# Optimization experiments

Measured on AMD Instinct MI355X. Metric: run time of the kernel, lower is better.

## Reference

```python
import jax, jax.numpy as jnp
import numpy as np

H = 1024  # hidden_size


def setup_inputs() -> dict:
    key = jax.random.key(0)
    ks = jax.random.split(key, 8)
    B, S = 32, 2048
    scale_w = 1.0 / np.sqrt(H)
    scale_u = 1.0 / np.sqrt(2 * H)
    return {
        "encoder_annotations": jax.random.normal(ks[0], (B, S, 2 * H), dtype=jnp.float32),
        "decoder_prev_hidden": jax.random.normal(ks[1], (1, B, H), dtype=jnp.float32),
        "W_w": jax.random.uniform(ks[2], (H, H), jnp.float32, -scale_w, scale_w),
        "W_b": jax.random.uniform(ks[3], (H,), jnp.float32, -scale_w, scale_w),
        "U_w": jax.random.uniform(ks[4], (H, 2 * H), jnp.float32, -scale_u, scale_u),
        "U_b": jax.random.uniform(ks[5], (H,), jnp.float32, -scale_u, scale_u),
        "V_w": jax.random.uniform(ks[6], (1, H), jnp.float32, -scale_w, scale_w),
        "V_b": jax.random.uniform(ks[7], (1,), jnp.float32, -scale_w, scale_w),
    }


def reference(encoder_annotations, decoder_prev_hidden, W_w, W_b, U_w, U_b, V_w, V_b):
    # decoder_prev_hidden: [1, B, H] -> [B, 1, H]
    dh = jnp.transpose(decoder_prev_hidden, (1, 0, 2))
    # W(dh): [B, 1, H]; U(enc): [B, S, H]; broadcast add over S
    wq = jnp.einsum("boh,kh->bok", dh, W_w) + W_b
    uk = jnp.einsum("bsd,kd->bsk", encoder_annotations, U_w) + U_b
    act = jnp.tanh(wq + uk)  # [B, S, H]
    # V(act): [B, S, 1] -> scores [B, 1, S]
    scores = (jnp.einsum("bsh,oh->bso", act, V_w) + V_b).transpose(0, 2, 1)
    weights = jax.nn.softmax(scores, axis=2)  # [B, 1, S]
    context = jnp.einsum("bos,sd->bod", weights[:, 0:1].squeeze(1)[:, None, :].squeeze(1)[:, None, :], encoder_annotations) if False else jnp.matmul(weights, encoder_annotations)  # [B, 1, 2H]
    return context
```

## Files before the change

kernel.cpp:

```cpp
#include <hip/hip_runtime.h>
#include <hip/hip_bf16.h>

#define H_  1024
#define B_  32
#define S_  2048
#define K2_ 2048

typedef __attribute__((ext_vector_type(8))) short short8;
typedef __attribute__((ext_vector_type(4))) float floatx4;

__device__ __forceinline__ unsigned short f2bf(float x) {
    unsigned int u = __float_as_uint(x);
    u += 0x7fffu + ((u >> 16) & 1u);
    return (unsigned short)(u >> 16);
}

__device__ __forceinline__ float fast_tanh(float x) {
    float e = __expf(2.0f * x);
    return 1.0f - 2.0f / (e + 1.0f);
}

__global__ __launch_bounds__(256)
void wq_k(const float* __restrict__ dh, const float* __restrict__ Ww,
          const float* __restrict__ Wb, const float* __restrict__ Ub,
          float* __restrict__ wqbuf)
{
    const int b = blockIdx.x;
    const int tid = threadIdx.x;
    __shared__ float dhs[H_];
    for (int h = tid; h < H_; h += 256) dhs[h] = dh[b * H_ + h];
    __syncthreads();
    for (int n = tid; n < H_; n += 256) {
        const float4* row = (const float4*)(Ww + (size_t)n * H_);
        float acc = 0.f;
        #pragma unroll 4
        for (int h4 = 0; h4 < H_ / 4; h4++) {
            float4 wv = row[h4];
            acc += wv.x * dhs[h4 * 4 + 0] + wv.y * dhs[h4 * 4 + 1]
                 + wv.z * dhs[h4 * 4 + 2] + wv.w * dhs[h4 * 4 + 3];
        }
        wqbuf[b * H_ + n] = acc + Wb[n] + Ub[n];
    }
}

__global__ __launch_bounds__(256)
void gemm_scores(const float* __restrict__ enc, const float* __restrict__ Uw,
                 const float* __restrict__ wqbuf, const float* __restrict__ Vw,
                 float* __restrict__ partial)
{
    const int b   = blockIdx.z;
    const int mt  = blockIdx.x;
    const int nt  = blockIdx.y;
    const int tid = threadIdx.x;
    const int wave = tid >> 6;
    const int lane = tid & 63;

    __shared__ unsigned short As[128][32];
    __shared__ unsigned short Bs[128][32];
    __shared__ float sc[2][128];

    const float* Ab = enc + ((size_t)b * S_ + (size_t)mt * 128) * K2_;
    const float* Bb = Uw + (size_t)nt * 128 * K2_;

    floatx4 acc[4][4];
    #pragma unroll
    for (int i = 0; i < 4; i++)
        #pragma unroll
        for (int j = 0; j < 4; j++)
            acc[i][j] = (floatx4){0.f, 0.f, 0.f, 0.f};

    const int wm  = (wave & 1) * 64;
    const int wn  = (wave >> 1) * 64;
    const int l15 = lane & 15;
    const int kq  = (lane >> 4) * 8;

    for (int ks = 0; ks < K2_; ks += 32) {
        #pragma unroll
        for (int i = 0; i < 4; i++) {
            int lin = tid + 256 * i;
            int row = lin >> 3;
            int kk  = (lin & 7) << 2;
            float4 av = *(const float4*)(Ab + (size_t)row * K2_ + ks + kk);
            float4 bv = *(const float4*)(Bb + (size_t)row * K2_ + ks + kk);
            ushort4 a4 = { f2bf(av.x), f2bf(av.y), f2bf(av.z), f2bf(av.w) };
            ushort4 b4 = { f2bf(bv.x), f2bf(bv.y), f2bf(bv.z), f2bf(bv.w) };
            *(ushort4*)&As[row][kk] = a4;
            *(ushort4*)&Bs[row][kk] = b4;
        }
        __syncthreads();

        short8 af[4], bfr[4];
        #pragma unroll
        for (int t = 0; t < 4; t++) {
            af[t]  = *(const short8*)&As[wm + t * 16 + l15][kq];
            bfr[t] = *(const short8*)&Bs[wn + t * 16 + l15][kq];
        }
        #pragma unroll
        for (int tm = 0; tm < 4; tm++)
            #pragma unroll
            for (int tn = 0; tn < 4; tn++)
                acc[tm][tn] = __builtin_amdgcn_mfma_f32_16x16x32_bf16(
                    af[tm], bfr[tn], acc[tm][tn], 0, 0, 0);
        __syncthreads();
    }

    float rs[4][4];
    #pragma unroll
    for (int tm = 0; tm < 4; tm++)
        #pragma unroll
        for (int r = 0; r < 4; r++) rs[tm][r] = 0.f;

    #pragma unroll
    for (int tn = 0; tn < 4; tn++) {
        int ng = nt * 128 + wn + tn * 16 + l15;
        float vw = Vw[ng];
        float wv = wqbuf[b * H_ + ng];
        #pragma unroll
        for (int tm = 0; tm < 4; tm++)
            #pragma unroll
            for (int r = 0; r < 4; r++)
                rs[tm][r] += vw * fast_tanh(acc[tm][tn][r] + wv);
    }
    #pragma unroll
    for (int tm = 0; tm < 4; tm++)
        #pragma unroll
        for (int r = 0; r < 4; r++) {
            float v = rs[tm][r];
            v += __shfl_xor(v, 1, 64);
            v += __shfl_xor(v, 2, 64);
            v += __shfl_xor(v, 4, 64);
            v += __shfl_xor(v, 8, 64);
            rs[tm][r] = v;
        }
    if (l15 == 0) {
        int q = lane >> 4;
        #pragma unroll
        for (int tm = 0; tm < 4; tm++)
            #pragma unroll
            for (int r = 0; r < 4; r++)
                sc[wave >> 1][wm + tm * 16 + q * 4 + r] = rs[tm][r];
    }
    __syncthreads();
    if (tid < 128)
        partial[(size_t)(b * 8 + nt) * S_ + mt * 128 + tid] = sc[0][tid] + sc[1][tid];
}

__global__ __launch_bounds__(256)
void softmax_k(const float* __restrict__ partial, float* __restrict__ weights)
{
    const int b = blockIdx.x;
    const int tid = threadIdx.x;
    __shared__ float scores[S_];
    __shared__ float redm[4], reds[4];

    for (int s = tid; s < S_; s += 256) {
        float v = 0.f;
        #pragma unroll
        for (int nt = 0; nt < 8; nt++) v += partial[(size_t)(b * 8 + nt) * S_ + s];
        scores[s] = v;
    }
    __syncthreads();

    float m = -1e30f;
    for (int s = tid; s < S_; s += 256) m = fmaxf(m, scores[s]);
    #pragma unroll
    for (int off = 32; off > 0; off >>= 1) m = fmaxf(m, __shfl_xor(m, off, 64));
    if ((tid & 63) == 0) redm[tid >> 6] = m;
    __syncthreads();
    m = fmaxf(fmaxf(redm[0], redm[1]), fmaxf(redm[2], redm[3]));

    float sum = 0.f;
    for (int s = tid; s < S_; s += 256) {
        float e = __expf(scores[s] - m);
        scores[s] = e;
        sum += e;
    }
    #pragma unroll
    for (int off = 32; off > 0; off >>= 1) sum += __shfl_xor(sum, off, 64);
    if ((tid & 63) == 0) reds[tid >> 6] = sum;
    __syncthreads();
    sum = reds[0] + reds[1] + reds[2] + reds[3];
    float inv = 1.0f / sum;
    for (int s = tid; s < S_; s += 256) weights[b * S_ + s] = scores[s] * inv;
}

__global__ __launch_bounds__(256)
void context_k(const float* __restrict__ enc, const float* __restrict__ weights,
               float* __restrict__ out)
{
    const int b = blockIdx.y;
    const int d = blockIdx.x * 256 + threadIdx.x;
    const int tid = threadIdx.x;
    __shared__ float w[S_];
    for (int s = tid; s < S_; s += 256) w[s] = weights[b * S_ + s];
    __syncthreads();

    const float* e = enc + (size_t)b * S_ * K2_ + d;
    float a0 = 0.f, a1 = 0.f, a2 = 0.f, a3 = 0.f;
    for (int s = 0; s < S_; s += 4) {
        a0 += w[s + 0] * e[(size_t)(s + 0) * K2_];
        a1 += w[s + 1] * e[(size_t)(s + 1) * K2_];
        a2 += w[s + 2] * e[(size_t)(s + 2) * K2_];
        a3 += w[s + 3] * e[(size_t)(s + 3) * K2_];
    }
    out[b * K2_ + d] = (a0 + a1) + (a2 + a3);
}

extern "C" void kernel_launch(void* const* d_in, const int* in_sizes, int n_in,
                              void* d_out, int out_size, void* d_ws, size_t ws_size,
                              hipStream_t stream)
{
    const float* enc = (const float*)d_in[0];
    const float* dh  = (const float*)d_in[1];
    const float* Ww  = (const float*)d_in[2];
    const float* Wb  = (const float*)d_in[3];
    const float* Uw  = (const float*)d_in[4];
    const float* Ub  = (const float*)d_in[5];
    const float* Vw  = (const float*)d_in[6];
    float* out = (float*)d_out;

    float* wqbuf   = (float*)d_ws;
    float* partial = wqbuf + B_ * H_;
    float* weights = partial + B_ * 8 * S_;

    wq_k<<<dim3(B_), dim3(256), 0, stream>>>(dh, Ww, Wb, Ub, wqbuf);
    gemm_scores<<<dim3(16, 8, B_), dim3(256), 0, stream>>>(enc, Uw, wqbuf, Vw, partial);
    softmax_k<<<dim3(B_), dim3(256), 0, stream>>>(partial, weights);
    context_k<<<dim3(8, B_), dim3(256), 0, stream>>>(enc, weights, out);
}
```

Baseline: 1.436 ms.

## Pre-convert operands to bf16, load via direct global-to-LDS, split context over S

Adds a pass that converts the encoder annotations and U weights to bf16 in workspace, then runs the score GEMM on bf16 inputs, loading tiles straight into LDS with global_load_lds. This removes the per-block fp32 loads and conversions, which were repeated across the 8 N-tiles. The context kernel is split over S chunks with float4 loads and a separate reduction kernel, giving more parallelism, and wq_k gets a wider grid. The trade-off is an extra full pass over the encoder (read fp32, write bf16), larger workspace needs, and a fallback to the old fp32 path when the workspace is too small.

```diff
diff --git a/kernel.cpp b/kernel.cpp
--- a/kernel.cpp
+++ b/kernel.cpp
@@ -8,6 +8,7 @@
 
 typedef __attribute__((ext_vector_type(8))) short short8;
 typedef __attribute__((ext_vector_type(4))) float floatx4;
+typedef __attribute__((ext_vector_type(8))) unsigned short ushortx8;
 
 __device__ __forceinline__ unsigned short f2bf(float x) {
     unsigned int u = __float_as_uint(x);
@@ -20,33 +21,154 @@
     return 1.0f - 2.0f / (e + 1.0f);
 }
 
+__device__ __forceinline__ void gload_lds16(const void* g, void* l) {
+    __builtin_amdgcn_global_load_lds(
+        (const __attribute__((address_space(1))) unsigned int*)g,
+        (__attribute__((address_space(3))) unsigned int*)l, 16, 0, 0);
+}
+
+__global__ __launch_bounds__(256)
+void cvt_bf16_k(const float* __restrict__ in, unsigned short* __restrict__ out, long long n8)
+{
+    long long i = (long long)blockIdx.x * 256 + threadIdx.x;
+    long long stride = (long long)gridDim.x * 256;
+    for (; i < n8; i += stride) {
+        const float4* p = (const float4*)in + i * 2;
+        float4 a = p[0], b = p[1];
+        ushortx8 o = { f2bf(a.x), f2bf(a.y), f2bf(a.z), f2bf(a.w),
+                       f2bf(b.x), f2bf(b.y), f2bf(b.z), f2bf(b.w) };
+        *(ushortx8*)(out + i * 8) = o;
+    }
+}
+
 __global__ __launch_bounds__(256)
 void wq_k(const float* __restrict__ dh, const float* __restrict__ Ww,
           const float* __restrict__ Wb, const float* __restrict__ Ub,
           float* __restrict__ wqbuf)
 {
-    const int b = blockIdx.x;
+    const int b = blockIdx.y;
+    const int n = blockIdx.x * 256 + threadIdx.x;
     const int tid = threadIdx.x;
     __shared__ float dhs[H_];
     for (int h = tid; h < H_; h += 256) dhs[h] = dh[b * H_ + h];
     __syncthreads();
-    for (int n = tid; n < H_; n += 256) {
-        const float4* row = (const float4*)(Ww + (size_t)n * H_);
-        float acc = 0.f;
-        #pragma unroll 4
-        for (int h4 = 0; h4 < H_ / 4; h4++) {
-            float4 wv = row[h4];
-            acc += wv.x * dhs[h4 * 4 + 0] + wv.y * dhs[h4 * 4 + 1]
-                 + wv.z * dhs[h4 * 4 + 2] + wv.w * dhs[h4 * 4 + 3];
-        }
-        wqbuf[b * H_ + n] = acc + Wb[n] + Ub[n];
-    }
-}
-
-__global__ __launch_bounds__(256)
-void gemm_scores(const float* __restrict__ enc, const float* __restrict__ Uw,
-                 const float* __restrict__ wqbuf, const float* __restrict__ Vw,
-                 float* __restrict__ partial)
+    const float4* row = (const float4*)(Ww + (size_t)n * H_);
+    float acc = 0.f;
+    #pragma unroll 4
+    for (int h4 = 0; h4 < H_ / 4; h4++) {
+        float4 wv = row[h4];
+        acc += wv.x * dhs[h4 * 4 + 0] + wv.y * dhs[h4 * 4 + 1]
+             + wv.z * dhs[h4 * 4 + 2] + wv.w * dhs[h4 * 4 + 3];
+    }
+    wqbuf[b * H_ + n] = acc + Wb[n] + Ub[n];
+}
+
+__global__ __launch_bounds__(256)
+void gemm_scores_bf16(const unsigned short* __restrict__ encb,
+                      const unsigned short* __restrict__ Uwb,
+                      const float* __restrict__ wqbuf, const float* __restrict__ Vw,
+                      float* __restrict__ partial)
+{
+    const int b   = blockIdx.z;
+    const int mt  = blockIdx.x;
+    const int nt  = blockIdx.y;
+    const int tid = threadIdx.x;
+    const int wave = tid >> 6;
+    const int lane = tid & 63;
+
+    __shared__ unsigned short As[128 * 32];
+    __shared__ unsigned short Bs[128 * 32];
+    __shared__ float sc[2][128];
+
+    const unsigned short* Ag = encb + ((size_t)b * S_ + (size_t)mt * 128) * K2_;
+    const unsigned short* Bg = Uwb + (size_t)nt * 128 * K2_;
+
+    floatx4 acc[4][4];
+    #pragma unroll
+    for (int i = 0; i < 4; i++)
+        #pragma unroll
+        for (int j = 0; j < 4; j++)
+            acc[i][j] = (floatx4){0.f, 0.f, 0.f, 0.f};
+
+    const int wm  = (wave & 1) * 64;
+    const int wn  = (wave >> 1) * 64;
+    const int l15 = lane & 15;
+    const int kq  = (lane >> 4) * 8;
+
+    const int r0 = lane >> 2;
+    const int ke = (lane & 3) * 8;
+    const unsigned short* aptr = Ag + (size_t)(wave * 32 + r0) * K2_ + ke;
+    const unsigned short* bptr = Bg + (size_t)(wave * 32 + r0) * K2_ + ke;
+    unsigned short* AldsA = As + wave * 1024;
+    unsigned short* AldsB = Bs + wave * 1024;
+
+    for (int ks = 0; ks < K2_; ks += 32) {
+        gload_lds16(aptr + ks,             AldsA);
+        gload_lds16(aptr + 16 * K2_ + ks,  AldsA + 512);
+        gload_lds16(bptr + ks,             AldsB);
+        gload_lds16(bptr + 16 * K2_ + ks,  AldsB + 512);
+        __syncthreads();
+
+        short8 af[4], bfr[4];
+        #pragma unroll
+        for (int t = 0; t < 4; t++) {
+            af[t]  = *(const short8*)&As[(wm + t * 16 + l15) * 32 + kq];
+            bfr[t] = *(const short8*)&Bs[(wn + t * 16 + l15) * 32 + kq];
+        }
+        #pragma unroll
+        for (int tm = 0; tm < 4; tm++)
+            #pragma unroll
+            for (int tn = 0; tn < 4; tn++)
+                acc[tm][tn] = __builtin_amdgcn_mfma_f32_16x16x32_bf16(
+                    af[tm], bfr[tn], acc[tm][tn], 0, 0, 0);
+        __syncthreads();
+    }
+
+    float rs[4][4];
+    #pragma unroll
+    for (int tm = 0; tm < 4; tm++)
+        #pragma unroll
+        for (int r = 0; r < 4; r++) rs[tm][r] = 0.f;
+
+    #pragma unroll
+    for (int tn = 0; tn < 4; tn++) {
+        int ng = nt * 128 + wn + tn * 16 + l15;
+        float vw = Vw[ng];
+        float wv = wqbuf[b * H_ + ng];
+        #pragma unroll
+        for (int tm = 0; tm < 4; tm++)
+            #pragma unroll
+            for (int r = 0; r < 4; r++)
+                rs[tm][r] += vw * fast_tanh(acc[tm][tn][r] + wv);
+    }
+    #pragma unroll
+    for (int tm = 0; tm < 4; tm++)
+        #pragma unroll
+        for (int r = 0; r < 4; r++) {
+            float v = rs[tm][r];
+            v += __shfl_xor(v, 1, 64);
+            v += __shfl_xor(v, 2, 64);
+            v += __shfl_xor(v, 4, 64);
+            v += __shfl_xor(v, 8, 64);
+            rs[tm][r] = v;
+        }
+    if (l15 == 0) {
+        int q = lane >> 4;
+        #pragma unroll
+        for (int tm = 0; tm < 4; tm++)
+            #pragma unroll
+            for (int r = 0; r < 4; r++)
+                sc[wave >> 1][wm + tm * 16 + q * 4 + r] = rs[tm][r];
+    }
+    __syncthreads();
+    if (tid < 128)
+        partial[(size_t)(b * 8 + nt) * S_ + mt * 128 + tid] = sc[0][tid] + sc[1][tid];
+}
+
+__global__ __launch_bounds__(256)
+void gemm_scores_f32(const float* __restrict__ enc, const float* __restrict__ Uw,
+                     const float* __restrict__ wqbuf, const float* __restrict__ Vw,
+                     float* __restrict__ partial)
 {
     const int b   = blockIdx.z;
     const int mt  = blockIdx.x;
@@ -185,25 +307,40 @@
 }
 
 __global__ __launch_bounds__(256)
-void context_k(const float* __restrict__ enc, const float* __restrict__ weights,
-               float* __restrict__ out)
-{
-    const int b = blockIdx.y;
-    const int d = blockIdx.x * 256 + threadIdx.x;
-    const int tid = threadIdx.x;
-    __shared__ float w[S_];
-    for (int s = tid; s < S_; s += 256) w[s] = weights[b * S_ + s];
-    __syncthreads();
-
-    const float* e = enc + (size_t)b * S_ * K2_ + d;
-    float a0 = 0.f, a1 = 0.f, a2 = 0.f, a3 = 0.f;
-    for (int s = 0; s < S_; s += 4) {
-        a0 += w[s + 0] * e[(size_t)(s + 0) * K2_];
-        a1 += w[s + 1] * e[(size_t)(s + 1) * K2_];
-        a2 += w[s + 2] * e[(size_t)(s + 2) * K2_];
-        a3 += w[s + 3] * e[(size_t)(s + 3) * K2_];
-    }
-    out[b * K2_ + d] = (a0 + a1) + (a2 + a3);
+void context2_k(const float* __restrict__ enc, const float* __restrict__ weights,
+                float* __restrict__ pctx)
+{
+    const int b = blockIdx.z, scnk = blockIdx.y, dblk = blockIdx.x;
+    const int tid = threadIdx.x;
+    __shared__ float w[256];
+    w[tid] = weights[b * S_ + scnk * 256 + tid];
+    __syncthreads();
+
+    const float4* e = (const float4*)(enc + ((size_t)b * S_ + scnk * 256) * K2_)
+                      + dblk * 256 + tid;
+    float4 a0 = {0,0,0,0}, a1 = {0,0,0,0};
+    #pragma unroll 4
+    for (int s = 0; s < 256; s += 2) {
+        float4 v0 = e[(size_t)s * 512];
+        float4 v1 = e[(size_t)(s + 1) * 512];
+        float w0 = w[s], w1 = w[s + 1];
+        a0.x += w0 * v0.x; a0.y += w0 * v0.y; a0.z += w0 * v0.z; a0.w += w0 * v0.w;
+        a1.x += w1 * v1.x; a1.y += w1 * v1.y; a1.z += w1 * v1.z; a1.w += w1 * v1.w;
+    }
+    float4 acc = { a0.x + a1.x, a0.y + a1.y, a0.z + a1.z, a0.w + a1.w };
+    float4* o = (float4*)(pctx + (size_t)(b * 8 + scnk) * K2_) + dblk * 256 + tid;
+    *o = acc;
+}
+
+__global__ __launch_bounds__(256)
+void ctx_reduce_k(const float* __restrict__ pctx, float* __restrict__ out)
+{
+    const int i = blockIdx.x * 256 + threadIdx.x;
+    const int b = i >> 11, d = i & 2047;
+    float s = 0.f;
+    #pragma unroll
+    for (int c = 0; c < 8; c++) s += pctx[(size_t)(b * 8 + c) * K2_ + d];
+    out[i] = s;
 }
 
 extern "C" void kernel_launch(void* const* d_in, const int* in_sizes, int n_in,
@@ -222,9 +359,25 @@
     float* wqbuf   = (float*)d_ws;
     float* partial = wqbuf + B_ * H_;
     float* weights = partial + B_ * 8 * S_;
-
-    wq_k<<<dim3(B_), dim3(256), 0, stream>>>(dh, Ww, Wb, Ub, wqbuf);
-    gemm_scores<<<dim3(16, 8, B_), dim3(256), 0, stream>>>(enc, Uw, wqbuf, Vw, partial);
+    float* pctx    = weights + B_ * S_;
+    size_t small_bytes = (size_t)(B_*H_ + B_*8*S_ + B_*S_ + B_*8*S_) * 4;
+    unsigned short* Uwb  = (unsigned short*)((char*)d_ws + small_bytes);
+    unsigned short* encb = Uwb + (size_t)H_ * K2_;
+    size_t need = small_bytes + (size_t)H_ * K2_ * 2 + (size_t)B_ * S_ * K2_ * 2;
+
+    wq_k<<<dim3(4, B_), dim3(256), 0, stream>>>(dh, Ww, Wb, Ub, wqbuf);
+
+    if (ws_size >= need) {
+        long long n8_enc = (long long)B_ * S_ * K2_ / 8;
+        long long n8_uw  = (long long)H_ * K2_ / 8;
+        cvt_bf16_k<<<dim3(8192), dim3(256), 0, stream>>>(enc, encb, n8_enc);
+        cvt_bf16_k<<<dim3(1024), dim3(256), 0, stream>>>(Uw, Uwb, n8_uw);
+        gemm_scores_bf16<<<dim3(16, 8, B_), dim3(256), 0, stream>>>(encb, Uwb, wqbuf, Vw, partial);
+    } else {
+        gemm_scores_f32<<<dim3(16, 8, B_), dim3(256), 0, stream>>>(enc, Uw, wqbuf, Vw, partial);
+    }
+
     softmax_k<<<dim3(B_), dim3(256), 0, stream>>>(partial, weights);
-    context_k<<<dim3(8, B_), dim3(256), 0, stream>>>(enc, weights, out);
-}
+    context2_k<<<dim3(2, 8, B_), dim3(256), 0, stream>>>(enc, weights, pctx);
+    ctx_reduce_k<<<dim3(256), dim3(256), 0, stream>>>(pctx, out);
+}
```

New measurement: 1.212 ms. 15.6% less time.
